# Kernel optimization log

Measured on AMD Instinct MI355X. Metric: run time of the kernel, lower is better.

The kernel has to match this reference:

```python
import jax, jax.numpy as jnp
import numpy as np
from jax import lax

B_SZ, L, D, N, R = 1, 4096, 768, 16, 48  # R = dt_rank = ceil(D/16)


def _soft_clamp(x, lo=1e-4, hi=10.0):
    center = (hi + lo) / 2.0
    half_range = (hi - lo) / 2.0
    return center + half_range * jnp.tanh((x - center) / half_range)


def setup_inputs() -> dict:
    key = jax.random.key(0)
    ks = jax.random.split(key, 6)
    x = jax.random.normal(ks[0], (B_SZ, L, D), jnp.float32)
    # A_log init: log(1..N) broadcast over D (HiPPO-style S4D-real init)
    A_log = jnp.log(jnp.broadcast_to(jnp.arange(1, N + 1, dtype=jnp.float32), (D, N)))
    D_param = jnp.ones((D,), jnp.float32)
    # lecun_normal kernels
    W_bc = jax.random.normal(ks[1], (D, 2 * N), jnp.float32) / np.sqrt(D).astype(np.float32)
    W_dt = jax.random.normal(ks[2], (D, R), jnp.float32) / np.sqrt(D).astype(np.float32)
    W_dtp = jax.random.normal(ks[3], (R, D), jnp.float32) / np.sqrt(R).astype(np.float32)
    # dt bias init: inverse-softplus of uniform(dt_min, dt_max)
    dt = jax.random.uniform(ks[4], (D,), jnp.float32, 0.001, 0.1)
    dt = jnp.clip(dt, 1e-4)
    b_dt = dt + jnp.log(-jnp.expm1(-dt))
    rms_scale = jnp.ones((D,), jnp.float32)  # RMSNorm learnable scale
    return {"x": x, "A_log": A_log, "D_param": D_param, "W_bc": W_bc,
            "W_dt": W_dt, "W_dtp": W_dtp, "b_dt": b_dt, "rms_scale": rms_scale}


def reference(x, A_log, D_param, W_bc, W_dt, W_dtp, b_dt, rms_scale):
    n = A_log.shape[1]
    A = -jnp.exp(A_log)                                   # (D, N)
    bc = x @ W_bc                                         # (B, L, 2N)
    B_sel, C_sel = bc[..., :n], bc[..., n:]               # (B, L, N) each
    # delta = softplus(dt_proj(x_dt)) -> RMSNorm -> soft_clamp  (tustin mode)
    delta = jax.nn.softplus((x @ W_dt) @ W_dtp + b_dt)    # (B, L, D)
    delta = delta * lax.rsqrt(jnp.mean(delta * delta, axis=-1, keepdims=True) + 1e-6) * rms_scale
    delta = _soft_clamp(delta, 1e-4, 10.0)
    # Bilinear (Tustin) discretization, all fp32 already
    dE = delta[..., None]                                 # (B, L, D, 1)
    half = 0.5 * dE * A                                   # (B, L, D, N)
    denom = 1.0 - half
    A_bar = (1.0 + half) / denom                          # (B, L, D, N)
    B_bar = jnp.sqrt(dE) * B_sel[:, :, None, :] / denom   # (B, L, D, N)
    # trapezoidal input averaging
    x_prev = jnp.concatenate([jnp.zeros_like(x[:, :1]), x[:, :-1]], axis=1)
    x_in = 0.5 * (x + x_prev)                             # (B, L, D)
    Bx = B_bar * x_in[..., None]                          # (B, L, D, N)

    def op(left, right):
        a_l, b_l = left
        a_r, b_r = right
        return (a_r * a_l, a_r * b_l + b_r)

    _, all_h = lax.associative_scan(op, (A_bar, Bx), axis=1)
    y = jnp.sum(C_sel[:, :, None, :] * all_h, axis=-1)    # (B, L, D)
    return y + D_param * x
```

## Files before the change

### kernel.cpp

```cpp
#include <hip/hip_runtime.h>
#include <math.h>

#define LSEQ 4096
#define DD 768
#define NST 16
#define RNK 48
#define TCH 32
#define NCH (LSEQ / TCH)
#define LTILE 8
#define XPAD 772

__device__ __forceinline__ float softplus_f(float z) {
    return fmaxf(z, 0.0f) + log1pf(expf(-fabsf(z)));
}

__device__ __forceinline__ float soft_clamp_f(float v) {
    const float ctr = 5.00005f;
    const float hr  = 4.99995f;
    const float inv_hr = 1.0f / 4.99995f;
    return ctr + hr * tanhf((v - ctr) * inv_hr);
}

__device__ __forceinline__ float wave_sum(float v) {
    #pragma unroll
    for (int m = 32; m >= 1; m >>= 1) v += __shfl_xor(v, m, 64);
    return v;
}

__global__ __launch_bounds__(512) void k_proj(
    const float* __restrict__ x, const float* __restrict__ W_bc,
    const float* __restrict__ W_dt, const float* __restrict__ W_dtp,
    const float* __restrict__ b_dt, const float* __restrict__ rms_scale,
    float* __restrict__ delta_out, float* __restrict__ bc_out)
{
    __shared__ __align__(16) float x_s[LTILE][XPAD];
    __shared__ __align__(16) float red[12][LTILE * 80];
    __shared__ __align__(16) float t_lds[LTILE][RNK];
    __shared__ float red2[8][LTILE];

    const int tid = threadIdx.x;
    const int l0  = blockIdx.x * LTILE;

    {
        const float4* xg = (const float4*)(x + (size_t)l0 * DD);
        #pragma unroll
        for (int k = 0; k < 3; ++k) {
            int idx = k * 512 + tid;
            int li = idx / 192;
            int j  = idx - li * 192;
            *(float4*)&x_s[li][j * 4] = xg[idx];
        }
    }
    __syncthreads();

    if (tid < 480) {
        const int q = tid % 40;
        const int p = tid / 40;
        const int j0 = 2 * q;
        const int dbase = p * 64;
        const int wstride = (j0 < RNK) ? RNK : 32;
        const float* Wb = (j0 < RNK) ? (W_dt + (size_t)dbase * RNK + j0)
                                     : (W_bc + (size_t)dbase * 32 + (j0 - RNK));
        float2 acc[LTILE];
        #pragma unroll
        for (int li = 0; li < LTILE; ++li) acc[li] = make_float2(0.f, 0.f);

        #pragma unroll 2
        for (int c = 0; c < 16; ++c) {
            const int i4 = c * 4;
            const float* Wp = Wb + (size_t)i4 * wstride;
            float2 wd0 = *(const float2*)(Wp);
            float2 wd1 = *(const float2*)(Wp + wstride);
            float2 wd2 = *(const float2*)(Wp + 2 * wstride);
            float2 wd3 = *(const float2*)(Wp + 3 * wstride);
            #pragma unroll
            for (int li = 0; li < LTILE; ++li) {
                float4 xv = *(const float4*)&x_s[li][dbase + i4];
                acc[li].x = fmaf(xv.x, wd0.x, acc[li].x);
                acc[li].y = fmaf(xv.x, wd0.y, acc[li].y);
                acc[li].x = fmaf(xv.y, wd1.x, acc[li].x);
                acc[li].y = fmaf(xv.y, wd1.y, acc[li].y);
                acc[li].x = fmaf(xv.z, wd2.x, acc[li].x);
                acc[li].y = fmaf(xv.z, wd2.y, acc[li].y);
                acc[li].x = fmaf(xv.w, wd3.x, acc[li].x);
                acc[li].y = fmaf(xv.w, wd3.y, acc[li].y);
            }
        }
        #pragma unroll
        for (int li = 0; li < LTILE; ++li)
            *(float2*)&red[p][li * 80 + j0] = acc[li];
    }
    __syncthreads();

    for (int idx = tid; idx < LTILE * 80; idx += 512) {
        float s = 0.f;
        #pragma unroll
        for (int p = 0; p < 12; ++p) s += red[p][idx];
        int li = idx / 80, jj = idx - 80 * li;
        if (jj < RNK) t_lds[li][jj] = s;
        else          bc_out[(size_t)(l0 + li) * 32 + (jj - RNK)] = s;
    }
    __syncthreads();

    const int d0 = tid;
    const int d1 = tid + 512;
    const bool has2 = (tid < 256);

    float z0[LTILE], z1[LTILE];
    {
        float bb0 = b_dt[d0];
        float bb1 = has2 ? b_dt[d1] : 0.f;
        #pragma unroll
        for (int li = 0; li < LTILE; ++li) { z0[li] = bb0; z1[li] = bb1; }
    }
    #pragma unroll 2
    for (int r4 = 0; r4 < RNK; r4 += 4) {
        float w00 = W_dtp[(r4 + 0) * DD + d0];
        float w01 = W_dtp[(r4 + 1) * DD + d0];
        float w02 = W_dtp[(r4 + 2) * DD + d0];
        float w03 = W_dtp[(r4 + 3) * DD + d0];
        float w10 = has2 ? W_dtp[(r4 + 0) * DD + d1] : 0.f;
        float w11 = has2 ? W_dtp[(r4 + 1) * DD + d1] : 0.f;
        float w12 = has2 ? W_dtp[(r4 + 2) * DD + d1] : 0.f;
        float w13 = has2 ? W_dtp[(r4 + 3) * DD + d1] : 0.f;
        #pragma unroll
        for (int li = 0; li < LTILE; ++li) {
            float4 t4 = *(const float4*)&t_lds[li][r4];
            z0[li] = fmaf(t4.x, w00, z0[li]);
            z0[li] = fmaf(t4.y, w01, z0[li]);
            z0[li] = fmaf(t4.z, w02, z0[li]);
            z0[li] = fmaf(t4.w, w03, z0[li]);
            z1[li] = fmaf(t4.x, w10, z1[li]);
            z1[li] = fmaf(t4.y, w11, z1[li]);
            z1[li] = fmaf(t4.z, w12, z1[li]);
            z1[li] = fmaf(t4.w, w13, z1[li]);
        }
    }
    #pragma unroll
    for (int li = 0; li < LTILE; ++li) {
        z0[li] = softplus_f(z0[li]);
        z1[li] = has2 ? softplus_f(z1[li]) : 0.f;
    }
    const int wid = tid >> 6;
    const int lane = tid & 63;
    #pragma unroll
    for (int li = 0; li < LTILE; ++li) {
        float ss = wave_sum(z0[li] * z0[li] + z1[li] * z1[li]);
        if (lane == 0) red2[wid][li] = ss;
    }
    __syncthreads();
    {
        float rs0 = rms_scale[d0];
        float rs1 = has2 ? rms_scale[d1] : 0.f;
        #pragma unroll
        for (int li = 0; li < LTILE; ++li) {
            float tot = 0.f;
            #pragma unroll
            for (int k = 0; k < 8; ++k) tot += red2[k][li];
            float inv = rsqrtf(tot * (1.0f / DD) + 1e-6f);
            delta_out[(size_t)(l0 + li) * DD + d0] = soft_clamp_f(z0[li] * inv * rs0);
            if (has2)
                delta_out[(size_t)(l0 + li) * DD + d1] = soft_clamp_f(z1[li] * inv * rs1);
        }
    }
}

__global__ __launch_bounds__(256, 8) void k_scan1(
    const float* __restrict__ x, const float* __restrict__ delta,
    const float* __restrict__ bc, const float* __restrict__ A_log,
    float* __restrict__ Pbuf, float* __restrict__ Hbuf)
{
    __shared__ __align__(16) float xs[(TCH + 1) * 64];
    __shared__ __align__(16) float sqv[TCH * 64];
    __shared__ __align__(16) float bs[TCH * 16];

    const int tid = threadIdx.x;
    const int db  = blockIdx.x * 64;
    const int c   = blockIdx.y;
    const int l0  = c * TCH;

    for (int i = tid; i < (TCH + 1) * 16; i += 256) {
        int r = i >> 4, f = i & 15;
        int l = l0 - 1 + r;
        float4 v = (l >= 0) ? *(const float4*)&x[(size_t)l * DD + db + f * 4]
                            : make_float4(0.f, 0.f, 0.f, 0.f);
        *(float4*)&xs[r * 64 + f * 4] = v;
    }
    for (int i = tid; i < TCH * 16; i += 256) {
        int r = i >> 4, f = i & 15;
        float4 v = *(const float4*)&delta[(size_t)(l0 + r) * DD + db + f * 4];
        v.x = sqrtf(v.x); v.y = sqrtf(v.y); v.z = sqrtf(v.z); v.w = sqrtf(v.w);
        *(float4*)&sqv[r * 64 + f * 4] = v;
    }
    if (tid < TCH * 4) {
        int r = tid >> 2, f = tid & 3;
        *(float4*)&bs[r * 16 + f * 4] =
            *(const float4*)&bc[(size_t)(l0 + r) * 32 + f * 4];
    }

    const int lane = tid & 63;
    const int w    = tid >> 6;
    const int q    = lane >> 4;
    const int dlo  = (lane & 15) + w * 16;
    const int d    = db + dlo;

    float An[4];
    {
        float4 a = *(const float4*)&A_log[d * NST + q * 4];
        An[0] = -expf(a.x); An[1] = -expf(a.y);
        An[2] = -expf(a.z); An[3] = -expf(a.w);
    }
    __syncthreads();

    float h[4]  = {0.f, 0.f, 0.f, 0.f};
    float Pp[4] = {1.f, 1.f, 1.f, 1.f};
    float xprev = xs[dlo];

    #pragma unroll 4
    for (int ll = 0; ll < TCH; ++ll) {
        float xv = xs[(ll + 1) * 64 + dlo];
        float sq = sqv[ll * 64 + dlo];
        float4 Bc = *(const float4*)&bs[ll * 16 + q * 4];

        float xin = 0.5f * (xv + xprev);
        xprev = xv;
        float c0 = 0.5f * sq * sq;
        float c1 = sq * xin;

        float dn0 = fmaf(-c0, An[0], 1.0f);
        float dn1 = fmaf(-c0, An[1], 1.0f);
        float dn2 = fmaf(-c0, An[2], 1.0f);
        float dn3 = fmaf(-c0, An[3], 1.0f);
        float m01 = dn0 * dn1, m23 = dn2 * dn3;
        float ip  = __builtin_amdgcn_rcpf(m01 * m23);
        float ip01 = ip * m23, ip23 = ip * m01;
        float iv0 = ip01 * dn1, iv1 = ip01 * dn0;
        float iv2 = ip23 * dn3, iv3 = ip23 * dn2;
        float t10 = 2.0f - dn0, t11 = 2.0f - dn1;
        float t12 = 2.0f - dn2, t13 = 2.0f - dn3;

        Pp[0] *= t10 * iv0;
        Pp[1] *= t11 * iv1;
        Pp[2] *= t12 * iv2;
        Pp[3] *= t13 * iv3;
        h[0] = fmaf(t10, h[0], c1 * Bc.x) * iv0;
        h[1] = fmaf(t11, h[1], c1 * Bc.y) * iv1;
        h[2] = fmaf(t12, h[2], c1 * Bc.z) * iv2;
        h[3] = fmaf(t13, h[3], c1 * Bc.w) * iv3;
    }
    #pragma unroll
    for (int n = 0; n < 4; ++n) {
        int idx = (c * NST + q * 4 + n) * DD + d;
        Pbuf[idx] = Pp[n];
        Hbuf[idx] = h[n];
    }
}

__global__ __launch_bounds__(64) void k_scan2(
    float* __restrict__ Pbuf, const float* __restrict__ Hbuf)
{
    const int s = blockIdx.x * 64 + threadIdx.x;
    const int d = s % DD;
    const int n = s / DD;
    const int stride = NST * DD;

    int idx = n * DD + d;
    int idx_pf = idx;
    float p[8], h[8];
    #pragma unroll
    for (int i = 0; i < 8; ++i) {
        p[i] = Pbuf[idx_pf];
        h[i] = Hbuf[idx_pf];
        idx_pf += stride;
    }

    float carry = 0.f;
    for (int g = 0; g < NCH / 8; ++g) {
        float pn[8], hn[8];
        if (g + 1 < NCH / 8) {
            #pragma unroll
            for (int i = 0; i < 8; ++i) {
                pn[i] = Pbuf[idx_pf];
                hn[i] = Hbuf[idx_pf];
                idx_pf += stride;
            }
        }
        #pragma unroll
        for (int i = 0; i < 8; ++i) {
            Pbuf[idx] = carry;
            carry = fmaf(p[i], carry, h[i]);
            idx += stride;
        }
        #pragma unroll
        for (int i = 0; i < 8; ++i) { p[i] = pn[i]; h[i] = hn[i]; }
    }
}

__global__ __launch_bounds__(256, 8) void k_scan3(
    const float* __restrict__ x, const float* __restrict__ delta,
    const float* __restrict__ bc, const float* __restrict__ A_log,
    const float* __restrict__ carryin, const float* __restrict__ D_param,
    float* __restrict__ out)
{
    __shared__ __align__(16) float xs[(TCH + 1) * 64];
    __shared__ __align__(16) float sqv[TCH * 64];
    __shared__ __align__(16) float bs[TCH * 32];

    const int tid = threadIdx.x;
    const int db  = blockIdx.x * 64;
    const int c   = blockIdx.y;
    const int l0  = c * TCH;

    for (int i = tid; i < (TCH + 1) * 16; i += 256) {
        int r = i >> 4, f = i & 15;
        int l = l0 - 1 + r;
        float4 v = (l >= 0) ? *(const float4*)&x[(size_t)l * DD + db + f * 4]
                            : make_float4(0.f, 0.f, 0.f, 0.f);
        *(float4*)&xs[r * 64 + f * 4] = v;
    }
    for (int i = tid; i < TCH * 16; i += 256) {
        int r = i >> 4, f = i & 15;
        float4 v = *(const float4*)&delta[(size_t)(l0 + r) * DD + db + f * 4];
        v.x = sqrtf(v.x); v.y = sqrtf(v.y); v.z = sqrtf(v.z); v.w = sqrtf(v.w);
        *(float4*)&sqv[r * 64 + f * 4] = v;
    }
    for (int i = tid; i < TCH * 8; i += 256) {
        int r = i >> 3, f = i & 7;
        *(float4*)&bs[r * 32 + f * 4] =
            *(const float4*)&bc[(size_t)(l0 + r) * 32 + f * 4];
    }

    const int lane = tid & 63;
    const int w    = tid >> 6;
    const int q    = lane >> 4;
    const int dlo  = (lane & 15) + w * 16;
    const int d    = db + dlo;

    float An[4];
    {
        float4 a = *(const float4*)&A_log[d * NST + q * 4];
        An[0] = -expf(a.x); An[1] = -expf(a.y);
        An[2] = -expf(a.z); An[3] = -expf(a.w);
    }
    float h[4];
    #pragma unroll
    for (int n = 0; n < 4; ++n)
        h[n] = carryin[(c * NST + q * 4 + n) * DD + d];
    const float Dp = D_param[d];

    __syncthreads();

    float xprev = xs[dlo];
    #pragma unroll 4
    for (int ll = 0; ll < TCH; ++ll) {
        float xv = xs[(ll + 1) * 64 + dlo];
        float sq = sqv[ll * 64 + dlo];
        float4 Bc = *(const float4*)&bs[ll * 32 + q * 4];
        float4 Cc = *(const float4*)&bs[ll * 32 + 16 + q * 4];

        float xin = 0.5f * (xv + xprev);
        xprev = xv;
        float c0 = 0.5f * sq * sq;
        float c1 = sq * xin;

        float dn0 = fmaf(-c0, An[0], 1.0f);
        float dn1 = fmaf(-c0, An[1], 1.0f);
        float dn2 = fmaf(-c0, An[2], 1.0f);
        float dn3 = fmaf(-c0, An[3], 1.0f);
        float m01 = dn0 * dn1, m23 = dn2 * dn3;
        float ip  = __builtin_amdgcn_rcpf(m01 * m23);
        float ip01 = ip * m23, ip23 = ip * m01;
        float iv0 = ip01 * dn1, iv1 = ip01 * dn0;
        float iv2 = ip23 * dn3, iv3 = ip23 * dn2;
        float t10 = 2.0f - dn0, t11 = 2.0f - dn1;
        float t12 = 2.0f - dn2, t13 = 2.0f - dn3;

        h[0] = fmaf(t10, h[0], c1 * Bc.x) * iv0;
        h[1] = fmaf(t11, h[1], c1 * Bc.y) * iv1;
        h[2] = fmaf(t12, h[2], c1 * Bc.z) * iv2;
        h[3] = fmaf(t13, h[3], c1 * Bc.w) * iv3;

        float y = h[0] * Cc.x;
        y = fmaf(h[1], Cc.y, y);
        y = fmaf(h[2], Cc.z, y);
        y = fmaf(h[3], Cc.w, y);

        y += __shfl_xor(y, 16, 64);
        y += __shfl_xor(y, 32, 64);
        if (q == 0)
            out[(size_t)(l0 + ll) * DD + d] = fmaf(Dp, xv, y);
    }
}

extern "C" void kernel_launch(void* const* d_in, const int* in_sizes, int n_in,
                              void* d_out, int out_size, void* d_ws, size_t ws_size,
                              hipStream_t stream) {
    const float* x         = (const float*)d_in[0];
    const float* A_log     = (const float*)d_in[1];
    const float* D_param   = (const float*)d_in[2];
    const float* W_bc      = (const float*)d_in[3];
    const float* W_dt      = (const float*)d_in[4];
    const float* W_dtp     = (const float*)d_in[5];
    const float* b_dt      = (const float*)d_in[6];
    const float* rms_scale = (const float*)d_in[7];
    float* out = (float*)d_out;

    float* ws    = (float*)d_ws;
    float* delta = ws;
    float* bcbuf = delta + (size_t)LSEQ * DD;
    float* Pbuf  = bcbuf + (size_t)LSEQ * 32;
    float* Hbuf  = Pbuf + (size_t)NCH * NST * DD;

    k_proj<<<LSEQ / LTILE, 512, 0, stream>>>(x, W_bc, W_dt, W_dtp, b_dt,
                                             rms_scale, delta, bcbuf);
    k_scan1<<<dim3(DD / 64, NCH), 256, 0, stream>>>(x, delta, bcbuf, A_log,
                                                    Pbuf, Hbuf);
    k_scan2<<<(DD * NST) / 64, 64, 0, stream>>>(Pbuf, Hbuf);
    k_scan3<<<dim3(DD / 64, NCH), 256, 0, stream>>>(x, delta, bcbuf, A_log,
                                                    Pbuf, D_param, out);
}
```

Measured before the change: 88.73 us.

## Move x@[W_dt|W_bc] projection to split-bf16 MFMA GEMM kernel

Splits the fused projection kernel in two. The first stage, x times the concatenated W_dt/W_bc weights, now runs as a separate GEMM on MFMA bf16 instructions, using a hi/lo bf16 split (three MFMAs per tile) to keep near-fp32 accuracy. A prep kernel converts and swizzles the weights into fragment layout on every call. The intermediate t is written to global memory and reloaded by the remaining dt_proj/RMSNorm kernel. This removes the LDS-staged scalar FMA loop and cross-group reduction, at the cost of two extra launches, an extra global round trip, and small 64-thread blocks.

```diff
diff --git a/kernel.cpp b/kernel.cpp
--- a/kernel.cpp
+++ b/kernel.cpp
@@ -8,7 +8,13 @@
 #define TCH 32
 #define NCH (LSEQ / TCH)
 #define LTILE 8
-#define XPAD 772
+#define NCOL 80
+#define KSTEPS 24
+#define NTILES 5
+#define WFRAG_N (KSTEPS * NTILES * 64 * 8)
+
+typedef __attribute__((ext_vector_type(8))) short bf16x8;
+typedef __attribute__((ext_vector_type(4))) float f32x4;
 
 __device__ __forceinline__ float softplus_f(float z) {
     return fmaxf(z, 0.0f) + log1pf(expf(-fabsf(z)));
@@ -27,79 +33,99 @@
     return v;
 }
 
-__global__ __launch_bounds__(512) void k_proj(
-    const float* __restrict__ x, const float* __restrict__ W_bc,
-    const float* __restrict__ W_dt, const float* __restrict__ W_dtp,
+__device__ __forceinline__ unsigned short rne_bf16(float v) {
+    unsigned u = __float_as_uint(v);
+    return (unsigned short)((u + 0x7FFFu + ((u >> 16) & 1u)) >> 16);
+}
+
+__global__ __launch_bounds__(256) void k_prep(
+    const float* __restrict__ W_dt, const float* __restrict__ W_bc,
+    unsigned short* __restrict__ wf_hi, unsigned short* __restrict__ wf_lo)
+{
+    int i = blockIdx.x * 256 + threadIdx.x;
+    if (i >= WFRAG_N) return;
+    int j  = i & 7;
+    int l  = (i >> 3) & 63;
+    int nk = i >> 9;
+    int n  = nk % NTILES;
+    int kk = nk / NTILES;
+    int k   = kk * 32 + (l >> 4) * 8 + j;
+    int col = n * 16 + (l & 15);
+    float v = (col < RNK) ? W_dt[k * RNK + col] : W_bc[k * 32 + (col - RNK)];
+    unsigned short h = rne_bf16(v);
+    float hf = __uint_as_float((unsigned)h << 16);
+    wf_hi[i] = h;
+    wf_lo[i] = rne_bf16(v - hf);
+}
+
+__global__ __launch_bounds__(64) void k_gemmA(
+    const float* __restrict__ x,
+    const unsigned short* __restrict__ wf_hi,
+    const unsigned short* __restrict__ wf_lo,
+    float* __restrict__ tbuf, float* __restrict__ bc_out)
+{
+    const int lane = threadIdx.x;
+    const int mt   = blockIdx.x;
+    const int row  = mt * 16 + (lane & 15);
+    const int ko   = (lane >> 4) * 8;
+
+    f32x4 acc[NTILES];
+    #pragma unroll
+    for (int n = 0; n < NTILES; ++n) acc[n] = (f32x4){0.f, 0.f, 0.f, 0.f};
+
+    #pragma unroll 2
+    for (int kk = 0; kk < KSTEPS; ++kk) {
+        const float* xp = x + (size_t)row * DD + kk * 32 + ko;
+        float4 xa = *(const float4*)xp;
+        float4 xb = *(const float4*)(xp + 4);
+        float va[8] = {xa.x, xa.y, xa.z, xa.w, xb.x, xb.y, xb.z, xb.w};
+        bf16x8 ah, al;
+        #pragma unroll
+        for (int j = 0; j < 8; ++j) {
+            unsigned short h = rne_bf16(va[j]);
+            float hf = __uint_as_float((unsigned)h << 16);
+            ah[j] = (short)h;
+            al[j] = (short)rne_bf16(va[j] - hf);
+        }
+        const int base = kk * (NTILES * 512) + lane * 8;
+        #pragma unroll
+        for (int n = 0; n < NTILES; ++n) {
+            bf16x8 bh = *(const bf16x8*)(wf_hi + base + n * 512);
+            bf16x8 bl = *(const bf16x8*)(wf_lo + base + n * 512);
+            acc[n] = __builtin_amdgcn_mfma_f32_16x16x32_bf16(al, bh, acc[n], 0, 0, 0);
+            acc[n] = __builtin_amdgcn_mfma_f32_16x16x32_bf16(ah, bl, acc[n], 0, 0, 0);
+            acc[n] = __builtin_amdgcn_mfma_f32_16x16x32_bf16(ah, bh, acc[n], 0, 0, 0);
+        }
+    }
+
+    const int r0 = mt * 16 + (lane >> 4) * 4;
+    const int cb = lane & 15;
+    #pragma unroll
+    for (int n = 0; n < 3; ++n)
+        #pragma unroll
+        for (int r = 0; r < 4; ++r)
+            tbuf[(size_t)(r0 + r) * RNK + n * 16 + cb] = acc[n][r];
+    #pragma unroll
+    for (int n = 3; n < 5; ++n)
+        #pragma unroll
+        for (int r = 0; r < 4; ++r)
+            bc_out[(size_t)(r0 + r) * 32 + (n - 3) * 16 + cb] = acc[n][r];
+}
+
+__global__ __launch_bounds__(512) void k_projB(
+    const float* __restrict__ tbuf, const float* __restrict__ W_dtp,
     const float* __restrict__ b_dt, const float* __restrict__ rms_scale,
-    float* __restrict__ delta_out, float* __restrict__ bc_out)
-{
-    __shared__ __align__(16) float x_s[LTILE][XPAD];
-    __shared__ __align__(16) float red[12][LTILE * 80];
+    float* __restrict__ delta_out)
+{
     __shared__ __align__(16) float t_lds[LTILE][RNK];
     __shared__ float red2[8][LTILE];
 
     const int tid = threadIdx.x;
     const int l0  = blockIdx.x * LTILE;
 
-    {
-        const float4* xg = (const float4*)(x + (size_t)l0 * DD);
-        #pragma unroll
-        for (int k = 0; k < 3; ++k) {
-            int idx = k * 512 + tid;
-            int li = idx / 192;
-            int j  = idx - li * 192;
-            *(float4*)&x_s[li][j * 4] = xg[idx];
-        }
-    }
-    __syncthreads();
-
-    if (tid < 480) {
-        const int q = tid % 40;
-        const int p = tid / 40;
-        const int j0 = 2 * q;
-        const int dbase = p * 64;
-        const int wstride = (j0 < RNK) ? RNK : 32;
-        const float* Wb = (j0 < RNK) ? (W_dt + (size_t)dbase * RNK + j0)
-                                     : (W_bc + (size_t)dbase * 32 + (j0 - RNK));
-        float2 acc[LTILE];
-        #pragma unroll
-        for (int li = 0; li < LTILE; ++li) acc[li] = make_float2(0.f, 0.f);
-
-        #pragma unroll 2
-        for (int c = 0; c < 16; ++c) {
-            const int i4 = c * 4;
-            const float* Wp = Wb + (size_t)i4 * wstride;
-            float2 wd0 = *(const float2*)(Wp);
-            float2 wd1 = *(const float2*)(Wp + wstride);
-            float2 wd2 = *(const float2*)(Wp + 2 * wstride);
-            float2 wd3 = *(const float2*)(Wp + 3 * wstride);
-            #pragma unroll
-            for (int li = 0; li < LTILE; ++li) {
-                float4 xv = *(const float4*)&x_s[li][dbase + i4];
-                acc[li].x = fmaf(xv.x, wd0.x, acc[li].x);
-                acc[li].y = fmaf(xv.x, wd0.y, acc[li].y);
-                acc[li].x = fmaf(xv.y, wd1.x, acc[li].x);
-                acc[li].y = fmaf(xv.y, wd1.y, acc[li].y);
-                acc[li].x = fmaf(xv.z, wd2.x, acc[li].x);
-                acc[li].y = fmaf(xv.z, wd2.y, acc[li].y);
-                acc[li].x = fmaf(xv.w, wd3.x, acc[li].x);
-                acc[li].y = fmaf(xv.w, wd3.y, acc[li].y);
-            }
-        }
-        #pragma unroll
-        for (int li = 0; li < LTILE; ++li)
-            *(float2*)&red[p][li * 80 + j0] = acc[li];
-    }
-    __syncthreads();
-
-    for (int idx = tid; idx < LTILE * 80; idx += 512) {
-        float s = 0.f;
-        #pragma unroll
-        for (int p = 0; p < 12; ++p) s += red[p][idx];
-        int li = idx / 80, jj = idx - 80 * li;
-        if (jj < RNK) t_lds[li][jj] = s;
-        else          bc_out[(size_t)(l0 + li) * 32 + (jj - RNK)] = s;
-    }
+    if (tid < 96)
+        *(float4*)&((float*)t_lds)[tid * 4] =
+            *(const float4*)&tbuf[(size_t)l0 * RNK + tid * 4];
     __syncthreads();
 
     const int d0 = tid;
@@ -410,9 +436,13 @@
     float* bcbuf = delta + (size_t)LSEQ * DD;
     float* Pbuf  = bcbuf + (size_t)LSEQ * 32;
     float* Hbuf  = Pbuf + (size_t)NCH * NST * DD;
-
-    k_proj<<<LSEQ / LTILE, 512, 0, stream>>>(x, W_bc, W_dt, W_dtp, b_dt,
-                                             rms_scale, delta, bcbuf);
+    float* tbuf  = Hbuf + (size_t)NCH * NST * DD;
+    unsigned short* wf_hi = (unsigned short*)(tbuf + (size_t)LSEQ * RNK);
+    unsigned short* wf_lo = wf_hi + WFRAG_N;
+
+    k_prep<<<(WFRAG_N + 255) / 256, 256, 0, stream>>>(W_dt, W_bc, wf_hi, wf_lo);
+    k_gemmA<<<LSEQ / 16, 64, 0, stream>>>(x, wf_hi, wf_lo, tbuf, bcbuf);
+    k_projB<<<LSEQ / LTILE, 512, 0, stream>>>(tbuf, W_dtp, b_dt, rms_scale, delta);
     k_scan1<<<dim3(DD / 64, NCH), 256, 0, stream>>>(x, delta, bcbuf, A_log,
                                                     Pbuf, Hbuf);
     k_scan2<<<(DD * NST) / 64, 64, 0, stream>>>(Pbuf, Hbuf);
```

Result: slower. 132.9 us (+49.8%).
